# Kernel optimization log

Hardware: AMD Instinct MI355X
Metric: run time of the kernel (lower is better)

Reference implementation:

```python
import jax, jax.numpy as jnp
import numpy as np

NB, NLOC, DIN, DOUT = 4, 4096, 512, 512
NTYPES, TEBD = 128, 128
N_EXPERTS, TOP_K = 8, 2  # share_expert = 0 -> routed_experts = 8, routed_top_k = 2


def setup_inputs() -> dict:
    key = jax.random.key(0)
    k = jax.random.split(key, 6)
    return {
        "x": jax.random.normal(k[0], (NB, NLOC, DIN), dtype=jnp.float32),
        "type_embeddings": jax.random.normal(k[1], (NTYPES, TEBD), dtype=jnp.float32),
        "atom_types": jax.random.randint(k[2], (NB, NLOC), 0, NTYPES, dtype=jnp.int32),
        "Wg": jax.random.normal(k[3], (TEBD, N_EXPERTS), dtype=jnp.float32) / np.sqrt(TEBD),
        "We": jax.random.normal(k[4], (N_EXPERTS, DIN, DOUT), dtype=jnp.float32) / np.sqrt(DIN),
        "be": jax.random.normal(k[5], (N_EXPERTS, DOUT), dtype=jnp.float32) * 0.01,
    }


def reference(x, type_embeddings, atom_types, Wg, We, be):
    # --- route: gate on type embeddings, then index per atom (MD-continuous) ---
    logits = type_embeddings @ Wg                       # [ntypes, E]
    top_vals, top_idx = jax.lax.top_k(logits, TOP_K)    # [ntypes, K]
    weights = jax.nn.softmax(top_vals, axis=-1)         # softmax over selected logits
    atom_w = weights[atom_types]                        # [nb, nloc, K]
    atom_i = top_idx[atom_types]                        # [nb, nloc, K]

    # scatter-add top-k weights into dense per-expert weights (matches scatter_add_)
    onehot = jax.nn.one_hot(atom_i, N_EXPERTS, dtype=x.dtype)   # [nb, nloc, K, E]
    per_expert_w = jnp.einsum("bnk,bnke->bne", atom_w, onehot)  # [nb, nloc, E]

    # --- run all experts densely (the batched JIT-friendly path), then combine ---
    expert_out = jnp.tanh(jnp.einsum("bnd,edo->bneo", x, We) + be)  # [nb, nloc, E, dout]
    out = jnp.einsum("bne,bneo->bno", per_expert_w, expert_out)     # [nb, nloc, dout]
    return out
```

## Files before the change

### kernel.cpp

```cpp
#include <hip/hip_runtime.h>
#include <hip/hip_bf16.h>
#include <math.h>

typedef __bf16 bf16;
typedef __bf16 bf16x8 __attribute__((ext_vector_type(8)));
typedef float  f32x4  __attribute__((ext_vector_type(4)));

#define NTOK   16384
#define DIN    512
#define DOUT   512
#define NTYPES 128
#define TEBD   128
#define NEXP   8
#define NPAIR  64
#define MAXTILE 192

#define WS_HPART   0
#define WS_ROUTE_W 32768
#define WS_PAIR    33792
#define WS_CNTP    34304
#define WS_NTILE   34816
#define WS_TMAP    35328
#define WS_RMAP    37888
#define WS_WGT     (WS_RMAP + MAXTILE * 128 * 4)
#define WS_XB      (WS_WGT + MAXTILE * 128 * 8)
#define WS_WET     (WS_XB + (size_t)NTOK * DIN * 2)

#define GLOAD_LDS16(g, l)                                                     \
  __builtin_amdgcn_global_load_lds(                                           \
      (const __attribute__((address_space(1))) void*)(g),                     \
      (__attribute__((address_space(3))) void*)(l), 16, 0, 0)

__global__ void fused_prep_kernel(const float* __restrict__ x,
                                  const float* __restrict__ We,
                                  const int* __restrict__ atype,
                                  const float* __restrict__ emb,
                                  const float* __restrict__ Wg,
                                  int* __restrict__ hpart,
                                  float* __restrict__ route_w,
                                  int* __restrict__ pair_ws,
                                  bf16* __restrict__ xb,
                                  bf16* __restrict__ WeT) {
  int bx = blockIdx.x;
  int tid = threadIdx.x;
  if (bx < 64) {
    __shared__ int h[NTYPES];
    if (tid < NTYPES) h[tid] = 0;
    __syncthreads();
    int t = bx * 256 + tid;
    atomicAdd(&h[atype[t]], 1);
    __syncthreads();
    if (tid < NTYPES) hpart[tid * 64 + bx] = h[tid];
  } else if (bx == 64) {
    int t = tid;
    if (t >= NTYPES) return;
    const float* er = emb + (size_t)t * TEBD;
    float lg[NEXP];
#pragma unroll
    for (int e = 0; e < NEXP; ++e) lg[e] = 0.f;
    for (int j = 0; j < TEBD; ++j) {
      float ev = er[j];
#pragma unroll
      for (int e = 0; e < NEXP; ++e) lg[e] += ev * Wg[j * NEXP + e];
    }
    float v0 = -__builtin_inff(), v1 = -__builtin_inff();
    int i0 = 0, i1 = 0;
#pragma unroll
    for (int e = 0; e < NEXP; ++e) {
      float v = lg[e];
      if (v > v0) { v1 = v0; i1 = i0; v0 = v; i0 = e; }
      else if (v > v1) { v1 = v; i1 = e; }
    }
    float d = expf(v1 - v0);
    float inv = 1.f / (1.f + d);
    route_w[t * 2 + 0] = inv;
    route_w[t * 2 + 1] = d * inv;
    pair_ws[t] = i0 * 8 + i1;
  } else if (bx < 577) {
    __shared__ float tle[64][65];
    int b2 = bx - 65;
    int e = b2 >> 6;
    int rem = b2 & 63;
    int kt = (rem >> 3) * 64;
    int nt = (rem & 7) * 64;
    int col = tid & 63;
    int rq = tid >> 6;
#pragma unroll
    for (int r = 0; r < 16; ++r) {
      int row = rq * 16 + r;
      tle[row][col] = We[((size_t)e * DIN + kt + row) * DOUT + nt + col];
    }
    __syncthreads();
#pragma unroll
    for (int r = 0; r < 16; ++r) {
      int n = rq * 16 + r;
      WeT[((size_t)e * DOUT + nt + n) * DIN + kt + col] = (bf16)tle[col][n];
    }
  } else {
    size_t base = (size_t)(bx - 577) * 4096 + tid * 16;
    const float4* p = (const float4*)(x + base);
    float4 a0 = p[0], a1 = p[1], a2 = p[2], a3 = p[3];
    bf16x8 o0, o1;
    o0[0] = (bf16)a0.x; o0[1] = (bf16)a0.y; o0[2] = (bf16)a0.z; o0[3] = (bf16)a0.w;
    o0[4] = (bf16)a1.x; o0[5] = (bf16)a1.y; o0[6] = (bf16)a1.z; o0[7] = (bf16)a1.w;
    o1[0] = (bf16)a2.x; o1[1] = (bf16)a2.y; o1[2] = (bf16)a2.z; o1[3] = (bf16)a2.w;
    o1[4] = (bf16)a3.x; o1[5] = (bf16)a3.y; o1[6] = (bf16)a3.z; o1[7] = (bf16)a3.w;
    *(bf16x8*)(xb + base) = o0;
    *(bf16x8*)(xb + base + 8) = o1;
  }
}

__global__ void scan_place_kernel(const int* __restrict__ hpart,
                                  const int* __restrict__ pair_ws,
                                  const int* __restrict__ atype,
                                  const float* __restrict__ route_w,
                                  int* __restrict__ cnt_pair,
                                  int* __restrict__ ntile,
                                  int* __restrict__ tmap,
                                  int* __restrict__ row_map,
                                  float* __restrict__ wgt) {
  __shared__ int s_pair[NTYPES];
  __shared__ int s_myc[NTYPES];
  __shared__ int s_pos0[NTYPES];
  __shared__ int s_cnt[NPAIR];
  __shared__ int s_base[NPAIR];
  __shared__ int lc[NTYPES];
  int b = blockIdx.x;
  int tid = threadIdx.x;

  if (tid < NTYPES) {
    s_pair[tid] = pair_ws[tid];
    int tot = 0, pre = 0;
    const int* hp = hpart + tid * 64;
#pragma unroll 8
    for (int j = 0; j < 64; ++j) {
      int v = hp[j];
      tot += v;
      if (j < b) pre += v;
    }
    s_myc[tid] = tot;
    s_pos0[tid] = pre;
    lc[tid] = 0;
  }
  __syncthreads();

  if (tid < NPAIR) {
    int c = 0;
    for (int t = 0; t < NTYPES; ++t)
      if (s_pair[t] == tid) c += s_myc[t];
    s_cnt[tid] = c;
  }
  __syncthreads();

  if (tid < NPAIR) {
    int bb = 0, tb = 0;
    for (int j = 0; j < tid; ++j) {
      int nt_j = (s_cnt[j] + 127) >> 7;
      bb += nt_j << 7;
      tb += nt_j;
    }
    s_base[tid] = bb;
    if (b == 0) {
      cnt_pair[tid] = s_cnt[tid];
      int nt_l = (s_cnt[tid] + 127) >> 7;
      for (int i = 0; i < nt_l; ++i) {
        tmap[(tb + i) * 2 + 0] = tid;
        tmap[(tb + i) * 2 + 1] = i * 128;
      }
      for (int i = s_cnt[tid]; i < (nt_l << 7); ++i) row_map[bb + i] = 0;
      if (tid == NPAIR - 1) ntile[0] = tb + nt_l;
    }
  }
  __syncthreads();

  if (tid < NTYPES) {
    int p = s_pair[tid];
    int off = 0;
    for (int t = 0; t < tid; ++t)
      if (s_pair[t] == p) off += s_myc[t];
    s_pos0[tid] += s_base[p] + off;
  }
  __syncthreads();

  int t = b * 256 + tid;
  int ty = atype[t];
  int r = atomicAdd(&lc[ty], 1);
  int pos = s_pos0[ty] + r;
  row_map[pos] = t;
  ((float2*)wgt)[pos] = ((const float2*)route_w)[ty];
}

__global__ __launch_bounds__(256, 2) void moe_gemm_pair_kernel(
    const bf16* __restrict__ xb, const bf16* __restrict__ WeT,
    const float* __restrict__ be, const int* __restrict__ cnt_pair,
    const int* __restrict__ ntile, const int* __restrict__ tmap,
    const int* __restrict__ row_map, const float* __restrict__ wgt,
    float* __restrict__ out) {
  int nwork = ntile[0] * 8;
  int f = blockIdx.y * 8 + blockIdx.x;
  if (f >= nwork) return;
  int q = nwork >> 3, r = nwork & 7;
  int xcd = f & 7, idx = f >> 3;
  int L = (xcd < r ? xcd * (q + 1) : r * (q + 1) + (xcd - r) * q) + idx;
  int ti = L >> 3;
  int cx = L & 7;
  int list = tmap[ti * 2 + 0];
  int r0   = tmap[ti * 2 + 1];
  int e0 = list >> 3, e1 = list & 7;
  int nrow = cnt_pair[list] - r0;
  if (nrow > 128) nrow = 128;
  int c0 = cx * 64;
  int arow0 = ti * 128;

  __shared__ __align__(16) bf16 As[4][128 * 32];
  __shared__ __align__(16) bf16 B0s[4][64 * 32];
  __shared__ __align__(16) bf16 B1s[4][64 * 32];
  __shared__ int   tokS[128];
  __shared__ float w0S[128], w1S[128];
  __shared__ float be0S[64], be1S[64];

  int tid = threadIdx.x;
  int lane = tid & 63, w = tid >> 6;

  if (tid < 128) {
    int srow = (tid < nrow) ? tid : (nrow - 1);
    tokS[tid] = row_map[arow0 + srow];
    float2 ww = ((const float2*)wgt)[arow0 + srow];
    w0S[tid] = ww.x;
    w1S[tid] = ww.y;
    if (tid < 64) {
      be0S[tid] = be[e0 * DOUT + c0 + tid];
      be1S[tid] = be[e1 * DOUT + c0 + tid];
    }
  }
  __syncthreads();

  const bf16* srcA[2];
#pragma unroll
  for (int j = 0; j < 2; ++j) {
    int slot = w * 128 + j * 64 + lane;
    int row = slot >> 2, cs = slot & 3;
    int c = cs ^ ((row >> 1) & 3);
    srcA[j] = xb + (size_t)tokS[row] * DIN + c * 8;
  }
  const bf16* srcB0;
  const bf16* srcB1;
  {
    int slot = w * 64 + lane;
    int row = slot >> 2, cs = slot & 3;
    int c = cs ^ ((row >> 1) & 3);
    srcB0 = WeT + ((size_t)e0 * DOUT + c0 + row) * DIN + c * 8;
    srcB1 = WeT + ((size_t)e1 * DOUT + c0 + row) * DIN + c * 8;
  }

  auto stage = [&](int buf) {
#pragma unroll
    for (int j = 0; j < 2; ++j) {
      GLOAD_LDS16(srcA[j], &As[buf][(w * 128 + j * 64) * 8]);
      srcA[j] += 32;
    }
    GLOAD_LDS16(srcB0, &B0s[buf][w * 64 * 8]);
    GLOAD_LDS16(srcB1, &B1s[buf][w * 64 * 8]);
    srcB0 += 32;
    srcB1 += 32;
  };

  stage(0);
  stage(1);
  stage(2);

  f32x4 acc0[4][2], acc1[4][2];
#pragma unroll
  for (int mi = 0; mi < 4; ++mi)
#pragma unroll
    for (int ni = 0; ni < 2; ++ni) { acc0[mi][ni] = (f32x4)0.f; acc1[mi][ni] = (f32x4)0.f; }

  int wm = (w >> 1) * 64;
  int wn = (w & 1) * 32;
  int r16 = lane & 15, g16 = lane >> 4;

  int offA[4], offB[2];
#pragma unroll
  for (int i = 0; i < 4; ++i) {
    int rA = wm + i * 16 + r16;
    offA[i] = rA * 32 + (g16 ^ ((rA >> 1) & 3)) * 8;
  }
#pragma unroll
  for (int i = 0; i < 2; ++i) {
    int rB = wn + i * 16 + r16;
    offB[i] = rB * 32 + (g16 ^ ((rB >> 1) & 3)) * 8;
  }

#pragma unroll
  for (int t = 0; t < 16; ++t) {
    if (t < 14)      asm volatile("s_waitcnt vmcnt(8)" ::: "memory");
    else if (t == 14) asm volatile("s_waitcnt vmcnt(4)" ::: "memory");
    else              asm volatile("s_waitcnt vmcnt(0)" ::: "memory");
    __builtin_amdgcn_s_barrier();
    if (t + 3 < 16) stage((t + 3) & 3);

    int cur = t & 3;
    bf16x8 af[4], b0f[2], b1f[2];
#pragma unroll
    for (int i = 0; i < 4; ++i) af[i] = *(const bf16x8*)&As[cur][offA[i]];
#pragma unroll
    for (int i = 0; i < 2; ++i) b0f[i] = *(const bf16x8*)&B0s[cur][offB[i]];
#pragma unroll
    for (int i = 0; i < 2; ++i) b1f[i] = *(const bf16x8*)&B1s[cur][offB[i]];
    __builtin_amdgcn_s_setprio(1);
#pragma unroll
    for (int mi = 0; mi < 4; ++mi)
#pragma unroll
      for (int ni = 0; ni < 2; ++ni) {
        acc0[mi][ni] = __builtin_amdgcn_mfma_f32_16x16x32_bf16(
            af[mi], b0f[ni], acc0[mi][ni], 0, 0, 0);
        acc1[mi][ni] = __builtin_amdgcn_mfma_f32_16x16x32_bf16(
            af[mi], b1f[ni], acc1[mi][ni], 0, 0, 0);
      }
    __builtin_amdgcn_s_setprio(0);
  }

#pragma unroll
  for (int mi = 0; mi < 4; ++mi) {
#pragma unroll
    for (int ni = 0; ni < 2; ++ni) {
      f32x4 v0 = acc0[mi][ni];
      f32x4 v1 = acc1[mi][ni];
      int colLocal = wn + ni * 16 + r16;
      float bev0 = be0S[colLocal];
      float bev1 = be1S[colLocal];
#pragma unroll
      for (int r = 0; r < 4; ++r) {
        int lrow = wm + mi * 16 + g16 * 4 + r;
        if (lrow < nrow) {
          float x0 = fminf(9.f, fmaxf(-9.f, v0[r] + bev0)) * 2.885390082f;
          float x1 = fminf(9.f, fmaxf(-9.f, v1[r] + bev1)) * 2.885390082f;
          float e0v, e1v, invd;
          asm("v_exp_f32 %0, %1" : "=v"(e0v) : "v"(x0));
          asm("v_exp_f32 %0, %1" : "=v"(e1v) : "v"(x1));
          float d0 = e0v + 1.f, d1 = e1v + 1.f;
          asm("v_rcp_f32 %0, %1" : "=v"(invd) : "v"(d0 * d1));
          float t0 = (e0v - 1.f) * d1 * invd;
          float t1 = (e1v - 1.f) * d0 * invd;
          out[(size_t)tokS[lrow] * DOUT + c0 + colLocal] =
              t0 * w0S[lrow] + t1 * w1S[lrow];
        }
      }
    }
  }
}

extern "C" void kernel_launch(void* const* d_in, const int* in_sizes, int n_in,
                              void* d_out, int out_size, void* d_ws, size_t ws_size,
                              hipStream_t stream) {
  const float* x    = (const float*)d_in[0];
  const float* emb  = (const float*)d_in[1];
  const int*   aty  = (const int*)d_in[2];
  const float* Wg   = (const float*)d_in[3];
  const float* We   = (const float*)d_in[4];
  const float* be   = (const float*)d_in[5];
  float* out = (float*)d_out;

  char* ws = (char*)d_ws;
  int*   hpart     = (int*)(ws + WS_HPART);
  float* route_w   = (float*)(ws + WS_ROUTE_W);
  int*   pair_ws   = (int*)(ws + WS_PAIR);
  int*   cnt_pair  = (int*)(ws + WS_CNTP);
  int*   ntile     = (int*)(ws + WS_NTILE);
  int*   tmap      = (int*)(ws + WS_TMAP);
  int*   row_map   = (int*)(ws + WS_RMAP);
  float* wgt       = (float*)(ws + WS_WGT);
  bf16*  xb        = (bf16*)(ws + WS_XB);
  bf16*  WeT       = (bf16*)(ws + WS_WET);

  fused_prep_kernel<<<2625, 256, 0, stream>>>(x, We, aty, emb, Wg, hpart,
                                              route_w, pair_ws, xb, WeT);
  scan_place_kernel<<<64, 256, 0, stream>>>(hpart, pair_ws, aty, route_w,
                                            cnt_pair, ntile, tmap, row_map, wgt);
  moe_gemm_pair_kernel<<<dim3(8, MAXTILE), 256, 0, stream>>>(
      xb, WeT, be, cnt_pair, ntile, tmap, row_map, wgt, out);
}
```

Measured before the change: 72.21 us.

## Fuse fp32-to-bf16 conversion of x into GEMM A-tile loading

Drops the separate x-to-bf16 prep pass, which read 32MB of fp32 and wrote 16MB of bf16. The GEMM now loads fp32 x rows into registers, converts them to bf16 and writes them into LDS, with a two-set register double buffer. The wait counts are reworked to match. The cost is that each x row is read as fp32 by all 8 column blocks and by both experts of its pair, which doubles A-side global traffic and adds register pressure, VALU conversion and LDS-store work inside the main loop.

```diff
diff --git a/kernel.cpp b/kernel.cpp
--- a/kernel.cpp
+++ b/kernel.cpp
@@ -23,23 +23,20 @@
 #define WS_TMAP    35328
 #define WS_RMAP    37888
 #define WS_WGT     (WS_RMAP + MAXTILE * 128 * 4)
-#define WS_XB      (WS_WGT + MAXTILE * 128 * 8)
-#define WS_WET     (WS_XB + (size_t)NTOK * DIN * 2)
+#define WS_WET     (WS_WGT + MAXTILE * 128 * 8)
 
 #define GLOAD_LDS16(g, l)                                                     \
   __builtin_amdgcn_global_load_lds(                                           \
       (const __attribute__((address_space(1))) void*)(g),                     \
       (__attribute__((address_space(3))) void*)(l), 16, 0, 0)
 
-__global__ void fused_prep_kernel(const float* __restrict__ x,
-                                  const float* __restrict__ We,
+__global__ void fused_prep_kernel(const float* __restrict__ We,
                                   const int* __restrict__ atype,
                                   const float* __restrict__ emb,
                                   const float* __restrict__ Wg,
                                   int* __restrict__ hpart,
                                   float* __restrict__ route_w,
                                   int* __restrict__ pair_ws,
-                                  bf16* __restrict__ xb,
                                   bf16* __restrict__ WeT) {
   int bx = blockIdx.x;
   int tid = threadIdx.x;
@@ -76,7 +73,7 @@
     route_w[t * 2 + 0] = inv;
     route_w[t * 2 + 1] = d * inv;
     pair_ws[t] = i0 * 8 + i1;
-  } else if (bx < 577) {
+  } else {
     __shared__ float tle[64][65];
     int b2 = bx - 65;
     int e = b2 >> 6;
@@ -96,17 +93,6 @@
       int n = rq * 16 + r;
       WeT[((size_t)e * DOUT + nt + n) * DIN + kt + col] = (bf16)tle[col][n];
     }
-  } else {
-    size_t base = (size_t)(bx - 577) * 4096 + tid * 16;
-    const float4* p = (const float4*)(x + base);
-    float4 a0 = p[0], a1 = p[1], a2 = p[2], a3 = p[3];
-    bf16x8 o0, o1;
-    o0[0] = (bf16)a0.x; o0[1] = (bf16)a0.y; o0[2] = (bf16)a0.z; o0[3] = (bf16)a0.w;
-    o0[4] = (bf16)a1.x; o0[5] = (bf16)a1.y; o0[6] = (bf16)a1.z; o0[7] = (bf16)a1.w;
-    o1[0] = (bf16)a2.x; o1[1] = (bf16)a2.y; o1[2] = (bf16)a2.z; o1[3] = (bf16)a2.w;
-    o1[4] = (bf16)a3.x; o1[5] = (bf16)a3.y; o1[6] = (bf16)a3.z; o1[7] = (bf16)a3.w;
-    *(bf16x8*)(xb + base) = o0;
-    *(bf16x8*)(xb + base + 8) = o1;
   }
 }
 
@@ -191,7 +177,7 @@
 }
 
 __global__ __launch_bounds__(256, 2) void moe_gemm_pair_kernel(
-    const bf16* __restrict__ xb, const bf16* __restrict__ WeT,
+    const float* __restrict__ x, const bf16* __restrict__ WeT,
     const float* __restrict__ be, const int* __restrict__ cnt_pair,
     const int* __restrict__ ntile, const int* __restrict__ tmap,
     const int* __restrict__ row_map, const float* __restrict__ wgt,
@@ -235,13 +221,15 @@
   }
   __syncthreads();
 
-  const bf16* srcA[2];
+  const float* srcAf[2];
+  int ldsSlot[2];
 #pragma unroll
   for (int j = 0; j < 2; ++j) {
     int slot = w * 128 + j * 64 + lane;
     int row = slot >> 2, cs = slot & 3;
     int c = cs ^ ((row >> 1) & 3);
-    srcA[j] = xb + (size_t)tokS[row] * DIN + c * 8;
+    srcAf[j] = x + (size_t)tokS[row] * DIN + c * 8;
+    ldsSlot[j] = (w * 128 + j * 64 + lane) * 8;
   }
   const bf16* srcB0;
   const bf16* srcB1;
@@ -253,21 +241,45 @@
     srcB1 = WeT + ((size_t)e1 * DOUT + c0 + row) * DIN + c * 8;
   }
 
-  auto stage = [&](int buf) {
-#pragma unroll
-    for (int j = 0; j < 2; ++j) {
-      GLOAD_LDS16(srcA[j], &As[buf][(w * 128 + j * 64) * 8]);
-      srcA[j] += 32;
-    }
+  float4 aR[2][2][2];
+
+#define ISSUE_A(set)                                                          \
+  {                                                                           \
+    _Pragma("unroll") for (int j = 0; j < 2; ++j) {                           \
+      aR[set][j][0] = *(const float4*)(srcAf[j]);                             \
+      aR[set][j][1] = *(const float4*)(srcAf[j] + 4);                         \
+      srcAf[j] += 32;                                                         \
+    }                                                                         \
+  }
+#define WRITE_A(buf, set)                                                     \
+  {                                                                           \
+    _Pragma("unroll") for (int j = 0; j < 2; ++j) {                           \
+      float4 lo = aR[set][j][0], hi = aR[set][j][1];                          \
+      bf16x8 o;                                                               \
+      o[0] = (bf16)lo.x; o[1] = (bf16)lo.y;                                   \
+      o[2] = (bf16)lo.z; o[3] = (bf16)lo.w;                                   \
+      o[4] = (bf16)hi.x; o[5] = (bf16)hi.y;                                   \
+      o[6] = (bf16)hi.z; o[7] = (bf16)hi.w;                                   \
+      *(bf16x8*)&As[buf][ldsSlot[j]] = o;                                     \
+    }                                                                         \
+  }
+
+  auto stageB = [&](int buf) {
     GLOAD_LDS16(srcB0, &B0s[buf][w * 64 * 8]);
     GLOAD_LDS16(srcB1, &B1s[buf][w * 64 * 8]);
     srcB0 += 32;
     srcB1 += 32;
   };
 
-  stage(0);
-  stage(1);
-  stage(2);
+  ISSUE_A(0);
+  ISSUE_A(1);
+  stageB(0); stageB(1); stageB(2);
+  asm volatile("s_waitcnt vmcnt(10)" ::: "memory");
+  WRITE_A(0, 0);
+  ISSUE_A(0);
+  asm volatile("s_waitcnt vmcnt(10)" ::: "memory");
+  WRITE_A(1, 1);
+  ISSUE_A(1);
 
   f32x4 acc0[4][2], acc1[4][2];
 #pragma unroll
@@ -293,11 +305,18 @@
 
 #pragma unroll
   for (int t = 0; t < 16; ++t) {
-    if (t < 14)      asm volatile("s_waitcnt vmcnt(8)" ::: "memory");
-    else if (t == 14) asm volatile("s_waitcnt vmcnt(4)" ::: "memory");
+    if (t == 0)       asm volatile("s_waitcnt vmcnt(4)" ::: "memory");
+    else if (t == 1)  asm volatile("s_waitcnt vmcnt(6)" ::: "memory");
+    else if (t <= 12) asm volatile("s_waitcnt vmcnt(8)" ::: "memory");
+    else if (t == 13) asm volatile("s_waitcnt vmcnt(4)" ::: "memory");
+    else if (t == 14) asm volatile("s_waitcnt vmcnt(2)" ::: "memory");
     else              asm volatile("s_waitcnt vmcnt(0)" ::: "memory");
+    if (t <= 13) WRITE_A((t + 2) & 3, t & 1);
+    asm volatile("s_waitcnt lgkmcnt(0)" ::: "memory");
+    __builtin_amdgcn_sched_barrier(0);
     __builtin_amdgcn_s_barrier();
-    if (t + 3 < 16) stage((t + 3) & 3);
+    if (t <= 11) ISSUE_A(t & 1);
+    if (t <= 12) stageB((t + 3) & 3);
 
     int cur = t & 3;
     bf16x8 af[4], b0f[2], b1f[2];
@@ -319,6 +338,8 @@
       }
     __builtin_amdgcn_s_setprio(0);
   }
+#undef ISSUE_A
+#undef WRITE_A
 
 #pragma unroll
   for (int mi = 0; mi < 4; ++mi) {
@@ -370,13 +391,12 @@
   int*   tmap      = (int*)(ws + WS_TMAP);
   int*   row_map   = (int*)(ws + WS_RMAP);
   float* wgt       = (float*)(ws + WS_WGT);
-  bf16*  xb        = (bf16*)(ws + WS_XB);
   bf16*  WeT       = (bf16*)(ws + WS_WET);
 
-  fused_prep_kernel<<<2625, 256, 0, stream>>>(x, We, aty, emb, Wg, hpart,
-                                              route_w, pair_ws, xb, WeT);
+  fused_prep_kernel<<<577, 256, 0, stream>>>(We, aty, emb, Wg, hpart,
+                                             route_w, pair_ws, WeT);
   scan_place_kernel<<<64, 256, 0, stream>>>(hpart, pair_ws, aty, route_w,
                                             cnt_pair, ntile, tmap, row_map, wgt);
   moe_gemm_pair_kernel<<<dim3(8, MAXTILE), 256, 0, stream>>>(
-      xb, WeT, be, cnt_pair, ntile, tmap, row_map, wgt, out);
+      x, WeT, be, cnt_pair, ntile, tmap, row_map, wgt, out);
 }
```

Measured after the change: 77.39 us. 1.07x slower.

## Fold routing histogram, scan and placement into the prep kernel

Applied to the files above, without the earlier changes.

Drops the separate scan_place kernel and the per-block histogram partials. Each of the 64 routing blocks in the fused prep kernel now recomputes the gate logits and top-2 routing, and builds the full type histogram plus its own prefix by scanning all 16384 atom types. This removes one kernel launch and the global round-trip between the two dependent steps. The cost is redundant work: each placement block reads all atom types and recomputes the gate, with heavy shared atomics.

```diff
diff --git a/kernel.cpp b/kernel.cpp
--- a/kernel.cpp
+++ b/kernel.cpp
@@ -15,13 +15,10 @@
 #define NPAIR  64
 #define MAXTILE 192
 
-#define WS_HPART   0
-#define WS_ROUTE_W 32768
-#define WS_PAIR    33792
-#define WS_CNTP    34304
-#define WS_NTILE   34816
-#define WS_TMAP    35328
-#define WS_RMAP    37888
+#define WS_CNTP    0
+#define WS_NTILE   512
+#define WS_TMAP    1024
+#define WS_RMAP    4096
 #define WS_WGT     (WS_RMAP + MAXTILE * 128 * 4)
 #define WS_XB      (WS_WGT + MAXTILE * 128 * 8)
 #define WS_WET     (WS_XB + (size_t)NTOK * DIN * 2)
@@ -36,51 +33,19 @@
                                   const int* __restrict__ atype,
                                   const float* __restrict__ emb,
                                   const float* __restrict__ Wg,
-                                  int* __restrict__ hpart,
-                                  float* __restrict__ route_w,
-                                  int* __restrict__ pair_ws,
+                                  int* __restrict__ cnt_pair,
+                                  int* __restrict__ ntile,
+                                  int* __restrict__ tmap,
+                                  int* __restrict__ row_map,
+                                  float* __restrict__ wgt,
                                   bf16* __restrict__ xb,
                                   bf16* __restrict__ WeT) {
   int bx = blockIdx.x;
   int tid = threadIdx.x;
-  if (bx < 64) {
-    __shared__ int h[NTYPES];
-    if (tid < NTYPES) h[tid] = 0;
-    __syncthreads();
-    int t = bx * 256 + tid;
-    atomicAdd(&h[atype[t]], 1);
-    __syncthreads();
-    if (tid < NTYPES) hpart[tid * 64 + bx] = h[tid];
-  } else if (bx == 64) {
-    int t = tid;
-    if (t >= NTYPES) return;
-    const float* er = emb + (size_t)t * TEBD;
-    float lg[NEXP];
-#pragma unroll
-    for (int e = 0; e < NEXP; ++e) lg[e] = 0.f;
-    for (int j = 0; j < TEBD; ++j) {
-      float ev = er[j];
-#pragma unroll
-      for (int e = 0; e < NEXP; ++e) lg[e] += ev * Wg[j * NEXP + e];
-    }
-    float v0 = -__builtin_inff(), v1 = -__builtin_inff();
-    int i0 = 0, i1 = 0;
-#pragma unroll
-    for (int e = 0; e < NEXP; ++e) {
-      float v = lg[e];
-      if (v > v0) { v1 = v0; i1 = i0; v0 = v; i0 = e; }
-      else if (v > v1) { v1 = v; i1 = e; }
-    }
-    float d = expf(v1 - v0);
-    float inv = 1.f / (1.f + d);
-    route_w[t * 2 + 0] = inv;
-    route_w[t * 2 + 1] = d * inv;
-    pair_ws[t] = i0 * 8 + i1;
-  } else if (bx < 577) {
+  if (bx < 512) {
     __shared__ float tle[64][65];
-    int b2 = bx - 65;
-    int e = b2 >> 6;
-    int rem = b2 & 63;
+    int e = bx >> 6;
+    int rem = bx & 63;
     int kt = (rem >> 3) * 64;
     int nt = (rem & 7) * 64;
     int col = tid & 63;
@@ -96,8 +61,8 @@
       int n = rq * 16 + r;
       WeT[((size_t)e * DOUT + nt + n) * DIN + kt + col] = (bf16)tle[col][n];
     }
-  } else {
-    size_t base = (size_t)(bx - 577) * 4096 + tid * 16;
+  } else if (bx < 2560) {
+    size_t base = (size_t)(bx - 512) * 4096 + tid * 16;
     const float4* p = (const float4*)(x + base);
     float4 a0 = p[0], a1 = p[1], a2 = p[2], a3 = p[3];
     bf16x8 o0, o1;
@@ -107,87 +72,94 @@
     o1[4] = (bf16)a3.x; o1[5] = (bf16)a3.y; o1[6] = (bf16)a3.z; o1[7] = (bf16)a3.w;
     *(bf16x8*)(xb + base) = o0;
     *(bf16x8*)(xb + base + 8) = o1;
-  }
-}
-
-__global__ void scan_place_kernel(const int* __restrict__ hpart,
-                                  const int* __restrict__ pair_ws,
-                                  const int* __restrict__ atype,
-                                  const float* __restrict__ route_w,
-                                  int* __restrict__ cnt_pair,
-                                  int* __restrict__ ntile,
-                                  int* __restrict__ tmap,
-                                  int* __restrict__ row_map,
-                                  float* __restrict__ wgt) {
-  __shared__ int s_pair[NTYPES];
-  __shared__ int s_myc[NTYPES];
-  __shared__ int s_pos0[NTYPES];
-  __shared__ int s_cnt[NPAIR];
-  __shared__ int s_base[NPAIR];
-  __shared__ int lc[NTYPES];
-  int b = blockIdx.x;
-  int tid = threadIdx.x;
-
-  if (tid < NTYPES) {
-    s_pair[tid] = pair_ws[tid];
-    int tot = 0, pre = 0;
-    const int* hp = hpart + tid * 64;
-#pragma unroll 8
-    for (int j = 0; j < 64; ++j) {
-      int v = hp[j];
-      tot += v;
-      if (j < b) pre += v;
-    }
-    s_myc[tid] = tot;
-    s_pos0[tid] = pre;
-    lc[tid] = 0;
-  }
-  __syncthreads();
-
-  if (tid < NPAIR) {
-    int c = 0;
-    for (int t = 0; t < NTYPES; ++t)
-      if (s_pair[t] == tid) c += s_myc[t];
-    s_cnt[tid] = c;
-  }
-  __syncthreads();
-
-  if (tid < NPAIR) {
-    int bb = 0, tb = 0;
-    for (int j = 0; j < tid; ++j) {
-      int nt_j = (s_cnt[j] + 127) >> 7;
-      bb += nt_j << 7;
-      tb += nt_j;
-    }
-    s_base[tid] = bb;
-    if (b == 0) {
-      cnt_pair[tid] = s_cnt[tid];
-      int nt_l = (s_cnt[tid] + 127) >> 7;
-      for (int i = 0; i < nt_l; ++i) {
-        tmap[(tb + i) * 2 + 0] = tid;
-        tmap[(tb + i) * 2 + 1] = i * 128;
-      }
-      for (int i = s_cnt[tid]; i < (nt_l << 7); ++i) row_map[bb + i] = 0;
-      if (tid == NPAIR - 1) ntile[0] = tb + nt_l;
-    }
-  }
-  __syncthreads();
-
-  if (tid < NTYPES) {
-    int p = s_pair[tid];
-    int off = 0;
-    for (int t = 0; t < tid; ++t)
-      if (s_pair[t] == p) off += s_myc[t];
-    s_pos0[tid] += s_base[p] + off;
-  }
-  __syncthreads();
-
-  int t = b * 256 + tid;
-  int ty = atype[t];
-  int r = atomicAdd(&lc[ty], 1);
-  int pos = s_pos0[ty] + r;
-  row_map[pos] = t;
-  ((float2*)wgt)[pos] = ((const float2*)route_w)[ty];
+  } else {
+    __shared__ float s_w0[NTYPES], s_w1[NTYPES];
+    __shared__ int s_pair[NTYPES];
+    __shared__ int s_pre[NTYPES], s_tot[NTYPES];
+    __shared__ int s_cnt[NPAIR], s_base[NPAIR];
+    __shared__ int s_pos0[NTYPES];
+    __shared__ int lc[NTYPES];
+    int b = bx - 2560;
+
+    if (tid < NTYPES) {
+      const float* er = emb + (size_t)tid * TEBD;
+      float lg[NEXP];
+#pragma unroll
+      for (int e = 0; e < NEXP; ++e) lg[e] = 0.f;
+      for (int j = 0; j < TEBD; ++j) {
+        float ev = er[j];
+#pragma unroll
+        for (int e = 0; e < NEXP; ++e) lg[e] += ev * Wg[j * NEXP + e];
+      }
+      float v0 = -__builtin_inff(), v1 = -__builtin_inff();
+      int i0 = 0, i1 = 0;
+#pragma unroll
+      for (int e = 0; e < NEXP; ++e) {
+        float v = lg[e];
+        if (v > v0) { v1 = v0; i1 = i0; v0 = v; i0 = e; }
+        else if (v > v1) { v1 = v; i1 = e; }
+      }
+      float d = expf(v1 - v0);
+      float inv = 1.f / (1.f + d);
+      s_w0[tid] = inv;
+      s_w1[tid] = d * inv;
+      s_pair[tid] = i0 * 8 + i1;
+      s_pre[tid] = 0; s_tot[tid] = 0; lc[tid] = 0;
+    }
+    __syncthreads();
+
+    int lim = b * 256;
+    for (int i = tid; i < NTOK; i += 256) {
+      int ty = atype[i];
+      atomicAdd(&s_tot[ty], 1);
+      if (i < lim) atomicAdd(&s_pre[ty], 1);
+    }
+    __syncthreads();
+
+    if (tid < NPAIR) {
+      int c = 0;
+      for (int t = 0; t < NTYPES; ++t)
+        if (s_pair[t] == tid) c += s_tot[t];
+      s_cnt[tid] = c;
+    }
+    __syncthreads();
+    if (tid < NPAIR) {
+      int bb = 0, tb = 0;
+      for (int j = 0; j < tid; ++j) {
+        int nt_j = (s_cnt[j] + 127) >> 7;
+        bb += nt_j << 7;
+        tb += nt_j;
+      }
+      s_base[tid] = bb;
+      if (b == 0) {
+        cnt_pair[tid] = s_cnt[tid];
+        int nt_l = (s_cnt[tid] + 127) >> 7;
+        for (int i = 0; i < nt_l; ++i) {
+          tmap[(tb + i) * 2 + 0] = tid;
+          tmap[(tb + i) * 2 + 1] = i * 128;
+        }
+        for (int i = s_cnt[tid]; i < (nt_l << 7); ++i) row_map[bb + i] = 0;
+        if (tid == NPAIR - 1) ntile[0] = tb + nt_l;
+      }
+    }
+    __syncthreads();
+    if (tid < NTYPES) {
+      int p = s_pair[tid];
+      int off = 0;
+      for (int t = 0; t < tid; ++t)
+        if (s_pair[t] == p) off += s_tot[t];
+      s_pos0[tid] = s_base[p] + off + s_pre[tid];
+    }
+    __syncthreads();
+
+    int t = b * 256 + tid;
+    int ty = atype[t];
+    int r = atomicAdd(&lc[ty], 1);
+    int pos = s_pos0[ty] + r;
+    row_map[pos] = t;
+    float2 ww; ww.x = s_w0[ty]; ww.y = s_w1[ty];
+    ((float2*)wgt)[pos] = ww;
+  }
 }
 
 __global__ __launch_bounds__(256, 2) void moe_gemm_pair_kernel(
@@ -362,9 +334,6 @@
   float* out = (float*)d_out;
 
   char* ws = (char*)d_ws;
-  int*   hpart     = (int*)(ws + WS_HPART);
-  float* route_w   = (float*)(ws + WS_ROUTE_W);
-  int*   pair_ws   = (int*)(ws + WS_PAIR);
   int*   cnt_pair  = (int*)(ws + WS_CNTP);
   int*   ntile     = (int*)(ws + WS_NTILE);
   int*   tmap      = (int*)(ws + WS_TMAP);
@@ -373,10 +342,8 @@
   bf16*  xb        = (bf16*)(ws + WS_XB);
   bf16*  WeT       = (bf16*)(ws + WS_WET);
 
-  fused_prep_kernel<<<2625, 256, 0, stream>>>(x, We, aty, emb, Wg, hpart,
-                                              route_w, pair_ws, xb, WeT);
-  scan_place_kernel<<<64, 256, 0, stream>>>(hpart, pair_ws, aty, route_w,
-                                            cnt_pair, ntile, tmap, row_map, wgt);
+  fused_prep_kernel<<<2624, 256, 0, stream>>>(x, We, aty, emb, Wg, cnt_pair,
+                                              ntile, tmap, row_map, wgt, xb, WeT);
   moe_gemm_pair_kernel<<<dim3(8, MAXTILE), 256, 0, stream>>>(
       xb, WeT, be, cnt_pair, ntile, tmap, row_map, wgt, out);
 }
```

After: 88.44 us. +22.5%, slower.
